# Kernel optimization log

Hardware: AMD Instinct MI355X
Metric: run time of the kernel (lower is better)

The kernel has to match this reference:

```python
import jax, jax.numpy as jnp
import numpy as np
from jax import lax


def _conv(x, w, padding, groups=1):
    # NCHW / OIHW 2D conv, stride 1
    return lax.conv_general_dilated(
        x, w, window_strides=(1, 1), padding=padding,
        dimension_numbers=("NCHW", "OIHW", "NCHW"),
        feature_group_count=groups)


def setup_inputs() -> dict:
    key = jax.random.key(0)
    ks = jax.random.split(key, 5)
    B, C, H, W = 8, 192, 128, 128
    HEADS = 8
    rgb = jax.random.normal(ks[0], (B, C, H, W), dtype=jnp.float32)
    ir = jax.random.normal(ks[1], (B, C, H, W), dtype=jnp.float32)
    w_qkv = jax.random.normal(ks[2], (3 * C, C, 1, 1), dtype=jnp.float32) * 0.02
    w_dw = jax.random.normal(ks[3], (3 * C, 1, 3, 3), dtype=jnp.float32) * 0.02
    w_proj = jax.random.normal(ks[4], (C, C, 1, 1), dtype=jnp.float32) * 0.02
    temperature = jnp.ones((HEADS, 1, 1), dtype=jnp.float32)
    return {"rgb": rgb, "ir": ir, "w_qkv": w_qkv, "w_dw": w_dw,
            "w_proj": w_proj, "temperature": temperature}


def reference(rgb, ir, w_qkv, w_dw, w_proj, temperature):
    heads = temperature.shape[0]
    b, c, h, w = rgb.shape
    hd = c // heads  # per-head channel count

    def qkv(x):
        y = _conv(x, w_qkv, "VALID")                 # [b, 3c, h, w]
        y = _conv(y, w_dw, "SAME", groups=3 * c)      # depthwise 3x3
        q, k, v = jnp.split(y, 3, axis=1)
        rs = lambda t: t.reshape(b, heads, hd, h * w)  # b head c (h w)
        return rs(q), rs(k), rs(v)

    rq, rk, rv = qkv(rgb)
    iq, ik, iv = qkv(ir)

    # torch F.normalize(dim=-1): x / max(||x||_2, 1e-12)
    nrm = lambda t: t / jnp.maximum(jnp.linalg.norm(t, axis=-1, keepdims=True), 1e-12)
    rq, rk, iq, ik = nrm(rq), nrm(rk), nrm(iq), nrm(ik)

    # channel-wise (transposed) cross attention: [b,h,hd,hd] attn matrices
    attn_ir = jax.nn.softmax(jnp.einsum("bhcn,bhdn->bhcd", rq, ik) * temperature, axis=-1)
    attn_rgb = jax.nn.softmax(jnp.einsum("bhcn,bhdn->bhcd", iq, rk) * temperature, axis=-1)

    out_ir = jnp.einsum("bhcd,bhdn->bhcn", attn_ir, iv).reshape(b, c, h, w)
    out_rgb = jnp.einsum("bhcd,bhdn->bhcn", attn_rgb, rv).reshape(b, c, h, w)

    out_ir = _conv(out_ir, w_proj, "VALID")
    out_rgb = _conv(out_rgb, w_proj, "VALID")
    return out_rgb, out_ir
```

## Files before the change

### kernel.cpp

```cpp
#include <hip/hip_runtime.h>

#define N_PIX 16384
#define CC    192
#define C3    576
#define KK    192
#define HD    24
#define GSPLIT 32

typedef __attribute__((ext_vector_type(8))) short short8;
typedef __attribute__((ext_vector_type(4))) float f32x4;

__device__ __forceinline__ unsigned short f2bf(float x) {
    unsigned u = __float_as_uint(x);
    u += 0x7fff + ((u >> 16) & 1);
    return (unsigned short)(u >> 16);
}
__device__ __forceinline__ float bf2f(unsigned short s) {
    return __uint_as_float(((unsigned)s) << 16);
}
__device__ __forceinline__ int pack2(unsigned short lo, unsigned short hi) {
    return (int)(((unsigned)hi << 16) | (unsigned)lo);
}

__device__ __forceinline__ void g2l16(const unsigned short* g, unsigned short* l) {
    __builtin_amdgcn_global_load_lds(
        (const __attribute__((address_space(1))) void*)g,
        (__attribute__((address_space(3))) void*)l, 16, 0, 0);
}

__global__ __launch_bounds__(256) void cvt_f32_bf16(const float* __restrict__ src,
                                                    unsigned short* __restrict__ dst, int n4) {
    int i = blockIdx.x * 256 + threadIdx.x;
    if (i < n4) {
        float4 v = ((const float4*)src)[i];
        ushort4 o;
        o.x = f2bf(v.x); o.y = f2bf(v.y); o.z = f2bf(v.z); o.w = f2bf(v.w);
        ((ushort4*)dst)[i] = o;
    }
}

__global__ __launch_bounds__(512, 4) void qkv_mfma(const unsigned short* __restrict__ wbf,
                                                   const float* __restrict__ rgb,
                                                   const float* __restrict__ ir,
                                                   unsigned short* __restrict__ Ybf) {
    const int z = blockIdx.z;
    const float* xg = ((z >= 8) ? ir : rgb) + (long)(z & 7) * CC * N_PIX;
    unsigned short* y = Ybf + (long)z * C3 * N_PIX;
    const int m0 = blockIdx.x * 192, n0 = blockIdx.y * 128;

    __shared__ unsigned short As[2][192 * 64];
    __shared__ unsigned short Bs[2][128 * 64];

    const int tid  = threadIdx.x;
    const int wave = tid >> 6, lane = tid & 63;
    const int quad = lane >> 4, l15 = lane & 15;
    const int wr = wave >> 2, wc = wave & 3;

    f32x4 acc[6][2];
#pragma unroll
    for (int i = 0; i < 6; i++)
#pragma unroll
        for (int j = 0; j < 2; j++) acc[i][j] = (f32x4)0.f;

    const int nq = tid & 63, kq = tid >> 6;

    auto stageA = [&](int buf, int k0) {
#pragma unroll
        for (int s = 0; s < 3; s++) {
            int j = s * 8 + wave;
            int q = j * 64 + lane;
            int m = q >> 3, c = (q & 7) ^ (m & 7);
            g2l16(wbf + (long)(m0 + m) * KK + k0 + c * 8, &As[buf][j * 512]);
        }
    };

    float2 bv[8];
    auto loadB = [&](int k0) {
#pragma unroll
        for (int j = 0; j < 8; j++)
            bv[j] = *(const float2*)(xg + (long)(k0 + kq * 8 + j) * N_PIX + n0 + nq * 2);
    };
    auto writeB = [&](int buf) {
#pragma unroll
        for (int i = 0; i < 2; i++) {
            int n = nq * 2 + i;
            unsigned short us[8];
#pragma unroll
            for (int j = 0; j < 8; j++) us[j] = f2bf(i ? bv[j].y : bv[j].x);
            int4 pk = make_int4(pack2(us[0], us[1]), pack2(us[2], us[3]),
                                pack2(us[4], us[5]), pack2(us[6], us[7]));
            int c = kq ^ (n & 7);
            *(int4*)&Bs[buf][n * 64 + c * 8] = pk;
        }
    };

    loadB(0);
    stageA(0, 0);
    writeB(0);
    __syncthreads();

    int cur = 0;
    for (int it = 0; it < 3; ++it) {
        if (it < 2) {
            stageA(cur ^ 1, (it + 1) * 64);
            loadB((it + 1) * 64);
        }
        const unsigned short* A  = As[cur];
        const unsigned short* Bl = Bs[cur];
#pragma unroll
        for (int kk = 0; kk < 2; kk++) {
            short8 a[6], b[2];
#pragma unroll
            for (int mi = 0; mi < 6; mi++) {
                int r = wr * 96 + mi * 16 + l15;
                int c = (kk * 4 + quad) ^ (r & 7);
                a[mi] = *(const short8*)&A[r * 64 + c * 8];
            }
#pragma unroll
            for (int ni = 0; ni < 2; ni++) {
                int n = wc * 32 + ni * 16 + l15;
                int c = (kk * 4 + quad) ^ (n & 7);
                b[ni] = *(const short8*)&Bl[n * 64 + c * 8];
            }
#pragma unroll
            for (int mi = 0; mi < 6; mi++)
#pragma unroll
                for (int ni = 0; ni < 2; ni++)
                    acc[mi][ni] = __builtin_amdgcn_mfma_f32_16x16x32_bf16(a[mi], b[ni], acc[mi][ni], 0, 0, 0);
        }
        if (it < 2) writeB(cur ^ 1);
        __syncthreads();
        cur ^= 1;
    }

#pragma unroll
    for (int mi = 0; mi < 6; mi++)
#pragma unroll
        for (int ni = 0; ni < 2; ni++)
#pragma unroll
            for (int r = 0; r < 4; r++) {
                int row = m0 + wr * 96 + mi * 16 + quad * 4 + r;
                int col = n0 + wc * 32 + ni * 16 + l15;
                y[(long)row * N_PIX + col] = f2bf(acc[mi][ni][r]);
            }
}

__global__ __launch_bounds__(512, 2) void gram_mfma(const unsigned short* __restrict__ Zbf,
                                                    float* __restrict__ gpart) {
    const int ks = blockIdx.x;
    const int zp = blockIdx.y;
    const int which = zp >> 3, b = zp & 7;
    const int zq = which ? 8 + b : b;
    const int zk = which ? b : 8 + b;
    const unsigned short* Qg = Zbf + (long)zq * C3 * N_PIX;
    const unsigned short* Kg = Zbf + ((long)zk * C3 + CC) * N_PIX;

    __shared__ unsigned short Qs[2][192 * 64];
    __shared__ unsigned short Ks[2][192 * 64];

    const int tid  = threadIdx.x;
    const int wave = tid >> 6, lane = tid & 63;
    const int quad = lane >> 4, l15 = lane & 15;
    const int wr = wave >> 1, wc = wave & 1;

    f32x4 acc[3][6];
#pragma unroll
    for (int i = 0; i < 3; i++)
#pragma unroll
        for (int j = 0; j < 6; j++) acc[i][j] = (f32x4)0.f;

    const int base = ks * 512;

    auto stage = [&](int buf, int k0) {
#pragma unroll
        for (int s = 0; s < 3; s++) {
            int j = s * 8 + wave;
            int q = j * 64 + lane;
            int m = q >> 3, c = (q & 7) ^ (m & 7);
            g2l16(Qg + (long)m * N_PIX + k0 + c * 8, &Qs[buf][j * 512]);
            g2l16(Kg + (long)m * N_PIX + k0 + c * 8, &Ks[buf][j * 512]);
        }
    };

    stage(0, base);
    __syncthreads();
    int cur = 0;
    for (int it = 0; it < 8; ++it) {
        if (it < 7) stage(cur ^ 1, base + (it + 1) * 64);
        const unsigned short* Q = Qs[cur];
        const unsigned short* Kl = Ks[cur];
#pragma unroll
        for (int kk = 0; kk < 2; kk++) {
            short8 a[3], bf[6];
#pragma unroll
            for (int mi = 0; mi < 3; mi++) {
                int r = wr * 48 + mi * 16 + l15;
                int c = (kk * 4 + quad) ^ (r & 7);
                a[mi] = *(const short8*)&Q[r * 64 + c * 8];
            }
#pragma unroll
            for (int ni = 0; ni < 6; ni++) {
                int n = wc * 96 + ni * 16 + l15;
                int c = (kk * 4 + quad) ^ (n & 7);
                bf[ni] = *(const short8*)&Kl[n * 64 + c * 8];
            }
#pragma unroll
            for (int mi = 0; mi < 3; mi++)
#pragma unroll
                for (int ni = 0; ni < 6; ni++)
                    acc[mi][ni] = __builtin_amdgcn_mfma_f32_16x16x32_bf16(a[mi], bf[ni], acc[mi][ni], 0, 0, 0);
        }
        __syncthreads();
        cur ^= 1;
    }

#pragma unroll
    for (int mi = 0; mi < 3; mi++)
#pragma unroll
        for (int ni = 0; ni < 6; ni++)
#pragma unroll
            for (int r = 0; r < 4; r++) {
                int row = wr * 48 + mi * 16 + quad * 4 + r;
                int col = wc * 96 + ni * 16 + l15;
                int hr = row / 24, hc = col / 24;
                if (hr == hc)
                    gpart[(((long)zp * GSPLIT + ks) * 8 + hr) * 576 +
                          (row - hr * 24) * 24 + (col - hc * 24)] = acc[mi][ni][r];
            }
}

__device__ __forceinline__ void mfma_gemm_old(const unsigned short* __restrict__ Abf,
                                              const unsigned short* __restrict__ Bsrc,
                                              float* __restrict__ Cdst,
                                              int m0, int n0) {
    __shared__ unsigned short As[192][44];
    __shared__ unsigned short Bs[128][44];

    const int tid  = threadIdx.x;
    const int wave = tid >> 6, lane = tid & 63;
    const int quad = lane >> 4, l15 = lane & 15;
    const int wr = wave >> 2, wc = wave & 3;

    f32x4 acc[6][2];
#pragma unroll
    for (int i = 0; i < 6; i++)
#pragma unroll
        for (int j = 0; j < 2; j++) acc[i][j] = (f32x4)0.f;

    const int kg = tid & 7;
    const int n2 = tid >> 3;

    for (int k0 = 0; k0 < KK; k0 += 32) {
        {
            int row = tid >> 2, kc = (tid & 3) * 8;
            *(int4*)&As[row][kc] = *(const int4*)(Abf + (long)(m0 + row) * KK + k0 + kc);
            if (tid < 256) {
                int ch = tid + 512;
                int row2 = ch >> 2, kc2 = (ch & 3) * 8;
                *(int4*)&As[row2][kc2] = *(const int4*)(Abf + (long)(m0 + row2) * KK + k0 + kc2);
            }
        }
        {
            ushort2 v[4];
#pragma unroll
            for (int j = 0; j < 4; j++)
                v[j] = *(const ushort2*)(Bsrc + (long)(k0 + kg * 4 + j) * N_PIX + n0 + n2 * 2);
#pragma unroll
            for (int i = 0; i < 2; i++) {
                unsigned short us[4];
#pragma unroll
                for (int j = 0; j < 4; j++) us[j] = i ? v[j].y : v[j].x;
                int2 pk = make_int2(pack2(us[0], us[1]), pack2(us[2], us[3]));
                *(int2*)&Bs[n2 * 2 + i][kg * 4] = pk;
            }
        }
        __syncthreads();

        short8 a[6], b[2];
#pragma unroll
        for (int mi = 0; mi < 6; mi++)
            a[mi] = *(const short8*)&As[wr * 96 + mi * 16 + l15][quad * 8];
#pragma unroll
        for (int ni = 0; ni < 2; ni++)
            b[ni] = *(const short8*)&Bs[wc * 32 + ni * 16 + l15][quad * 8];
#pragma unroll
        for (int mi = 0; mi < 6; mi++)
#pragma unroll
            for (int ni = 0; ni < 2; ni++)
                acc[mi][ni] = __builtin_amdgcn_mfma_f32_16x16x32_bf16(a[mi], b[ni], acc[mi][ni], 0, 0, 0);
        __syncthreads();
    }

#pragma unroll
    for (int mi = 0; mi < 6; mi++)
#pragma unroll
        for (int ni = 0; ni < 2; ni++)
#pragma unroll
            for (int r = 0; r < 4; r++) {
                int row = m0 + wr * 96 + mi * 16 + quad * 4 + r;
                int col = n0 + wc * 32 + ni * 16 + l15;
                Cdst[(long)row * N_PIX + col] = acc[mi][ni][r];
            }
}

__global__ __launch_bounds__(512, 4) void out_mfma(const unsigned short* __restrict__ weff,
                                                   const unsigned short* __restrict__ Zbf,
                                                   float* __restrict__ out) {
    const int z = blockIdx.z;
    const unsigned short* V = Zbf + ((long)z * C3 + 2 * CC) * N_PIX;
    float* C = out + (long)z * CC * N_PIX;
    mfma_gemm_old(weff + (long)z * CC * CC, V, C, 0, blockIdx.x * 128);
}

__global__ __launch_bounds__(256) void dwconv3x3(const unsigned short* __restrict__ Ybf,
                                                 const float* __restrict__ wdw,
                                                 unsigned short* __restrict__ Zbf,
                                                 float* __restrict__ nrm) {
    const int z  = blockIdx.z;
    const int oc = blockIdx.y;
    const int idx = blockIdx.x * 256 + threadIdx.x;
    const int p0  = idx * 8;
    const int h   = p0 >> 7;
    const int w0  = p0 & 127;
    const int wq  = threadIdx.x & 15;
    const unsigned short* Yc = Ybf + ((long)z * C3 + oc) * N_PIX;

    float wk[9];
#pragma unroll
    for (int i = 0; i < 9; i++) wk[i] = wdw[oc * 9 + i];

    float f[3][8];
#pragma unroll
    for (int ry = 0; ry < 3; ry++) {
        const int hy = h + ry - 1;
        int4 raw = make_int4(0, 0, 0, 0);
        if (hy >= 0 && hy <= 127)
            raw = *(const int4*)(Yc + hy * 128 + w0);
        f[ry][0] = bf2f((unsigned short)(raw.x & 0xffff));
        f[ry][1] = bf2f((unsigned short)((unsigned)raw.x >> 16));
        f[ry][2] = bf2f((unsigned short)(raw.y & 0xffff));
        f[ry][3] = bf2f((unsigned short)((unsigned)raw.y >> 16));
        f[ry][4] = bf2f((unsigned short)(raw.z & 0xffff));
        f[ry][5] = bf2f((unsigned short)((unsigned)raw.z >> 16));
        f[ry][6] = bf2f((unsigned short)(raw.w & 0xffff));
        f[ry][7] = bf2f((unsigned short)((unsigned)raw.w >> 16));
    }

    float acc[8];
#pragma unroll
    for (int j = 0; j < 8; j++) acc[j] = 0.f;

#pragma unroll
    for (int ry = 0; ry < 3; ry++) {
        float l = __shfl_up(f[ry][7], 1);
        float r = __shfl_down(f[ry][0], 1);
        if (wq == 0)  l = 0.f;
        if (wq == 15) r = 0.f;
        const float wl = wk[ry * 3 + 0], wc = wk[ry * 3 + 1], wr = wk[ry * 3 + 2];
        acc[0] = fmaf(wl, l, acc[0]);
#pragma unroll
        for (int j = 1; j < 8; j++) acc[j] = fmaf(wl, f[ry][j - 1], acc[j]);
#pragma unroll
        for (int j = 0; j < 8; j++) acc[j] = fmaf(wc, f[ry][j], acc[j]);
#pragma unroll
        for (int j = 0; j < 7; j++) acc[j] = fmaf(wr, f[ry][j + 1], acc[j]);
        acc[7] = fmaf(wr, r, acc[7]);
    }

    ushort4 o[2];
    unsigned short* po = (unsigned short*)o;
#pragma unroll
    for (int j = 0; j < 8; j++) po[j] = f2bf(acc[j]);
    *(int4*)(Zbf + ((long)z * C3 + oc) * N_PIX + p0) = *(const int4*)o;

    __shared__ float red[4];
    float ss = 0.f;
#pragma unroll
    for (int j = 0; j < 8; j++) {
        float v = bf2f(po[j]);
        ss = fmaf(v, v, ss);
    }
#pragma unroll
    for (int off = 32; off > 0; off >>= 1)
        ss += __shfl_down(ss, off);
    if ((threadIdx.x & 63) == 0) red[threadIdx.x >> 6] = ss;
    __syncthreads();
    if (threadIdx.x == 0 && oc < 2 * CC)
        nrm[((long)z * (2 * CC) + oc) * 8 + blockIdx.x] = red[0] + red[1] + red[2] + red[3];
}

__global__ __launch_bounds__(256) void gram_reduce_softmax(const float* __restrict__ gpart,
                                                           const float* __restrict__ nrm,
                                                           const float* __restrict__ temperature,
                                                           float* __restrict__ P) {
    const int g = blockIdx.x;
    const int which = g >> 6, b = (g >> 3) & 7, head = g & 7;
    const int zp = which * 8 + b;
    const int zq = which ? 8 + b : b;
    const int zk = which ? b : 8 + b;
    __shared__ float Gs[576];
    __shared__ float invq[24], invk[24];

    const int t = threadIdx.x;
    for (int e = t; e < 576; e += 256) {
        float s = 0.f;
        for (int sp = 0; sp < GSPLIT; sp++)
            s += gpart[(((long)zp * GSPLIT + sp) * 8 + head) * 576 + e];
        Gs[e] = s;
    }
    if (t < 24) {
        float s = 0.f;
#pragma unroll
        for (int b8 = 0; b8 < 8; b8++)
            s += nrm[((long)zq * (2 * CC) + head * HD + t) * 8 + b8];
        invq[t] = 1.f / fmaxf(sqrtf(s), 1e-12f);
    } else if (t >= 32 && t < 56) {
        float s = 0.f;
#pragma unroll
        for (int b8 = 0; b8 < 8; b8++)
            s += nrm[((long)zk * (2 * CC) + CC + head * HD + (t - 32)) * 8 + b8];
        invk[t - 32] = 1.f / fmaxf(sqrtf(s), 1e-12f);
    }
    __syncthreads();
    if (t < 24) {
        const float temp = temperature[head];
        float row[24];
        float m = -1e30f;
#pragma unroll
        for (int d = 0; d < 24; d++) {
            row[d] = Gs[t * 24 + d] * invq[t] * invk[d] * temp;
            m = fmaxf(m, row[d]);
        }
        float ssum = 0.f;
#pragma unroll
        for (int d = 0; d < 24; d++) {
            row[d] = expf(row[d] - m);
            ssum += row[d];
        }
        const float inv = 1.f / ssum;
#pragma unroll
        for (int d = 0; d < 24; d++)
            P[(long)g * 576 + t * 24 + d] = row[d] * inv;
    }
}

__global__ __launch_bounds__(256) void build_weff(const float* __restrict__ wproj,
                                                  const float* __restrict__ P,
                                                  unsigned short* __restrict__ weff) {
    const int o = blockIdx.z, b = blockIdx.y;
    const int e = blockIdx.x * 256 + threadIdx.x;
    const int co = e / 192, col = e % 192;
    const int head = col / 24, d = col % 24;
    const int which = 1 - o;
    const float* Pp = P + (long)(which * 64 + b * 8 + head) * 576;
    const float* wp = wproj + co * 192 + head * 24;
    float acc = 0.f;
#pragma unroll
    for (int hc = 0; hc < 24; hc++)
        acc = fmaf(wp[hc], Pp[hc * 24 + d], acc);
    weff[((long)(o * 8 + b) * 192 + co) * 192 + col] = f2bf(acc);
}

extern "C" void kernel_launch(void* const* d_in, const int* in_sizes, int n_in,
                              void* d_out, int out_size, void* d_ws, size_t ws_size,
                              hipStream_t stream) {
    (void)in_sizes; (void)n_in; (void)out_size; (void)ws_size;
    const float* rgb    = (const float*)d_in[0];
    const float* ir     = (const float*)d_in[1];
    const float* w_qkv  = (const float*)d_in[2];
    const float* w_dw   = (const float*)d_in[3];
    const float* w_proj = (const float*)d_in[4];
    const float* temp   = (const float*)d_in[5];
    float* out = (float*)d_out;

    char* wsb = (char*)d_ws;
    unsigned short* Y_bf    = (unsigned short*)(wsb);
    unsigned short* Z_bf    = (unsigned short*)(wsb + 301989888L);
    float*          gpart   = (float*)(wsb);
    unsigned short* w_bf    = (unsigned short*)(wsb + 603979776L);
    unsigned short* weff_bf = (unsigned short*)(wsb + 604200960L);
    float*          nrm     = (float*)(wsb + 605380608L);
    float*          P       = (float*)(wsb + 607936512L);

    cvt_f32_bf16<<<108, 256, 0, stream>>>(w_qkv, w_bf, 27648);
    qkv_mfma<<<dim3(3, 128, 16), 512, 0, stream>>>(w_bf, rgb, ir, Y_bf);
    dwconv3x3<<<dim3(8, 576, 16), 256, 0, stream>>>(Y_bf, w_dw, Z_bf, nrm);
    gram_mfma<<<dim3(GSPLIT, 16), 512, 0, stream>>>(Z_bf, gpart);
    gram_reduce_softmax<<<128, 256, 0, stream>>>(gpart, nrm, temp, P);
    build_weff<<<dim3(144, 8, 2), 256, 0, stream>>>(w_proj, P, weff_bf);
    out_mfma<<<dim3(128, 1, 16), 512, 0, stream>>>(weff_bf, Z_bf, out);
}
```

Before: 673.0 us.

## Remap qkv GEMM blocks for XCD locality and hand-pipeline its K loop

The QKV 1x1-conv GEMM now runs on a flat 1D grid. Block ids are remapped so that consecutive ids (id & 7 selects the chunk) land on the same XCD, and the three M tiles that share an input pixel tile stay adjacent, which should improve L2 reuse of the fp32 activations. The three-step K loop is fully unrolled with explicit s_waitcnt vmcnt/lgkmcnt counts, raw s_barrier and sched_barrier. This lets the next stage's global loads stay in flight while MFMAs run, instead of relying on a full __syncthreads each iteration. The hand-written vmcnt(11) count is fragile: it depends on exactly how many memory instructions the compiler emits.

Result: slower. 689.7 us (+2.5%).

```diff
diff --git a/kernel.cpp b/kernel.cpp
--- a/kernel.cpp
+++ b/kernel.cpp
@@ -43,10 +43,15 @@
                                                    const float* __restrict__ rgb,
                                                    const float* __restrict__ ir,
                                                    unsigned short* __restrict__ Ybf) {
-    const int z = blockIdx.z;
+    const int id  = blockIdx.x;
+    const int nid = (id & 7) * 768 + (id >> 3);
+    const int m0  = (nid % 3) * 192;
+    const int r   = nid / 3;
+    const int n0  = (r & 127) * 128;
+    const int z   = r >> 7;
+
     const float* xg = ((z >= 8) ? ir : rgb) + (long)(z & 7) * CC * N_PIX;
     unsigned short* y = Ybf + (long)z * C3 * N_PIX;
-    const int m0 = blockIdx.x * 192, n0 = blockIdx.y * 128;
 
     __shared__ unsigned short As[2][192 * 64];
     __shared__ unsigned short Bs[2][128 * 64];
@@ -64,6 +69,12 @@
 
     const int nq = tid & 63, kq = tid >> 6;
 
+    float2 bv[8];
+    auto loadB = [&](int k0) {
+#pragma unroll
+        for (int j = 0; j < 8; j++)
+            bv[j] = *(const float2*)(xg + (long)(k0 + kq * 8 + j) * N_PIX + n0 + nq * 2);
+    };
     auto stageA = [&](int buf, int k0) {
 #pragma unroll
         for (int s = 0; s < 3; s++) {
@@ -73,13 +84,6 @@
             g2l16(wbf + (long)(m0 + m) * KK + k0 + c * 8, &As[buf][j * 512]);
         }
     };
-
-    float2 bv[8];
-    auto loadB = [&](int k0) {
-#pragma unroll
-        for (int j = 0; j < 8; j++)
-            bv[j] = *(const float2*)(xg + (long)(k0 + kq * 8 + j) * N_PIX + n0 + nq * 2);
-    };
     auto writeB = [&](int buf) {
 #pragma unroll
         for (int i = 0; i < 2; i++) {
@@ -93,28 +97,17 @@
             *(int4*)&Bs[buf][n * 64 + c * 8] = pk;
         }
     };
-
-    loadB(0);
-    stageA(0, 0);
-    writeB(0);
-    __syncthreads();
-
-    int cur = 0;
-    for (int it = 0; it < 3; ++it) {
-        if (it < 2) {
-            stageA(cur ^ 1, (it + 1) * 64);
-            loadB((it + 1) * 64);
-        }
-        const unsigned short* A  = As[cur];
-        const unsigned short* Bl = Bs[cur];
+    auto mfma_step = [&](int buf) {
+        const unsigned short* A  = As[buf];
+        const unsigned short* Bl = Bs[buf];
 #pragma unroll
         for (int kk = 0; kk < 2; kk++) {
             short8 a[6], b[2];
 #pragma unroll
             for (int mi = 0; mi < 6; mi++) {
-                int r = wr * 96 + mi * 16 + l15;
-                int c = (kk * 4 + quad) ^ (r & 7);
-                a[mi] = *(const short8*)&A[r * 64 + c * 8];
+                int rr = wr * 96 + mi * 16 + l15;
+                int c = (kk * 4 + quad) ^ (rr & 7);
+                a[mi] = *(const short8*)&A[rr * 64 + c * 8];
             }
 #pragma unroll
             for (int ni = 0; ni < 2; ni++) {
@@ -128,20 +121,46 @@
                 for (int ni = 0; ni < 2; ni++)
                     acc[mi][ni] = __builtin_amdgcn_mfma_f32_16x16x32_bf16(a[mi], b[ni], acc[mi][ni], 0, 0, 0);
         }
-        if (it < 2) writeB(cur ^ 1);
-        __syncthreads();
-        cur ^= 1;
-    }
+    };
+
+    loadB(0);
+    stageA(0, 0);
+    writeB(0);
+
+    loadB(64);
+    stageA(1, 64);
+    asm volatile("s_waitcnt vmcnt(11) lgkmcnt(0)" ::: "memory");
+    __builtin_amdgcn_s_barrier();
+    __builtin_amdgcn_sched_barrier(0);
+    mfma_step(0);
+    writeB(1);
+    asm volatile("s_waitcnt lgkmcnt(0)" ::: "memory");
+    __builtin_amdgcn_s_barrier();
+
+    loadB(128);
+    stageA(0, 128);
+    asm volatile("s_waitcnt vmcnt(11) lgkmcnt(0)" ::: "memory");
+    __builtin_amdgcn_s_barrier();
+    __builtin_amdgcn_sched_barrier(0);
+    mfma_step(1);
+    writeB(0);
+    asm volatile("s_waitcnt lgkmcnt(0)" ::: "memory");
+    __builtin_amdgcn_s_barrier();
+
+    asm volatile("s_waitcnt vmcnt(0) lgkmcnt(0)" ::: "memory");
+    __builtin_amdgcn_s_barrier();
+    __builtin_amdgcn_sched_barrier(0);
+    mfma_step(0);
 
 #pragma unroll
     for (int mi = 0; mi < 6; mi++)
 #pragma unroll
         for (int ni = 0; ni < 2; ni++)
 #pragma unroll
-            for (int r = 0; r < 4; r++) {
-                int row = m0 + wr * 96 + mi * 16 + quad * 4 + r;
+            for (int rr = 0; rr < 4; rr++) {
+                int row = m0 + wr * 96 + mi * 16 + quad * 4 + rr;
                 int col = n0 + wc * 32 + ni * 16 + l15;
-                y[(long)row * N_PIX + col] = f2bf(acc[mi][ni][r]);
+                y[(long)row * N_PIX + col] = f2bf(acc[mi][ni][rr]);
             }
 }
 
@@ -483,7 +502,7 @@
     float*          P       = (float*)(wsb + 607936512L);
 
     cvt_f32_bf16<<<108, 256, 0, stream>>>(w_qkv, w_bf, 27648);
-    qkv_mfma<<<dim3(3, 128, 16), 512, 0, stream>>>(w_bf, rgb, ir, Y_bf);
+    qkv_mfma<<<6144, 512, 0, stream>>>(w_bf, rgb, ir, Y_bf);
     dwconv3x3<<<dim3(8, 576, 16), 256, 0, stream>>>(Y_bf, w_dw, Z_bf, nrm);
     gram_mfma<<<dim3(GSPLIT, 16), 512, 0, stream>>>(Z_bf, gpart);
     gram_reduce_softmax<<<128, 256, 0, stream>>>(gpart, nrm, temp, P);
```
